# Optimization experiments

Hardware: AMD Instinct MI355X
Metric: run time of the kernel (lower is better)

The kernel has to match this reference:

```python
import jax, jax.numpy as jnp
import numpy as np

B, N, D, H = 2, 2048, 768, 12
HD = D // H  # 64


def apply_rotary_embed(x, thetas):
    # x: (..., N, HD), thetas: (N, HD) broadcast over leading dims
    x1, x2 = jnp.split(x, 2, axis=-1)
    x_rot = jnp.concatenate([-x2, x1], axis=-1)
    return x * jnp.cos(thetas) + x_rot * jnp.sin(thetas)


def setup_inputs() -> dict:
    key = jax.random.key(0)
    ks = jax.random.split(key, 5)
    s = 0.02
    return {
        "x": jax.random.normal(ks[0], (B, N, D), dtype=jnp.float32),
        "pos_embed": jax.random.normal(ks[1], (N, HD), dtype=jnp.float32),
        "Wqkv": jax.random.normal(ks[2], (3 * D, D), dtype=jnp.float32) * s,
        "Wproj": jax.random.normal(ks[3], (D, D), dtype=jnp.float32) * s,
        "bproj": jnp.zeros((D,), dtype=jnp.float32),
    }


def reference(x, pos_embed, Wqkv, Wproj, bproj):
    Bb, Nn, Dd = x.shape
    # fused QKV projection (torch Linear: x @ W.T), no bias
    qkv = jnp.einsum('bnd,ed->bne', x, Wqkv)                 # (B, N, 3D)
    qkv = qkv.reshape(Bb, Nn, 3, H, HD).transpose(2, 0, 3, 1, 4)  # (3, B, H, N, HD)
    q, k, v = qkv[0], qkv[1], qkv[2]
    # rotary embedding on q and k
    q = apply_rotary_embed(q, pos_embed)
    k = apply_rotary_embed(k, pos_embed)
    # scaled dot-product attention (non-causal, no mask, no dropout)
    scale = 1.0 / jnp.sqrt(jnp.asarray(HD, dtype=x.dtype))
    scores = jnp.einsum('bhqd,bhkd->bhqk', q, k) * scale     # (B, H, N, N)
    attn = jax.nn.softmax(scores, axis=-1)
    out = jnp.einsum('bhqk,bhkd->bhqd', attn, v)             # (B, H, N, HD)
    out = out.transpose(0, 2, 1, 3).reshape(Bb, Nn, Dd)      # (B, N, D)
    # output projection (with bias)
    return jnp.einsum('bnd,ed->bne', out, Wproj) + bproj
```

## Files before the change

kernel.cpp:

```cpp
#include <hip/hip_runtime.h>
#include <stdint.h>

typedef __attribute__((ext_vector_type(8))) short short8;
typedef __attribute__((ext_vector_type(4))) float floatx4;
typedef __attribute__((ext_vector_type(16))) float floatx16;
typedef __attribute__((ext_vector_type(4))) unsigned int uintx4;

#define BB 2
#define NN 2048
#define DD 768
#define HH 12
#define HDD 64
#define MM (BB*NN)

__device__ __forceinline__ unsigned short f2bf(float f) {
  unsigned int u = __builtin_bit_cast(unsigned int, f);
  u += 0x7fffu + ((u >> 16) & 1u);
  return (unsigned short)(u >> 16);
}
__device__ __forceinline__ float bf2f(unsigned short u) {
  unsigned int v = ((unsigned int)u) << 16;
  return __builtin_bit_cast(float, v);
}

__device__ __forceinline__ void gld16(const unsigned short* g, unsigned short* l) {
  __builtin_amdgcn_global_load_lds(
      (const __attribute__((address_space(1))) void*)g,
      (__attribute__((address_space(3))) void*)l, 16, 0, 0);
}

__device__ __forceinline__ unsigned int cvtpk_bf16(float a, float b) {
  unsigned int r;
  asm("v_cvt_pk_bf16_f32 %0, %1, %2" : "=v"(r) : "v"(a), "v"(b));
  return r;
}
__device__ __forceinline__ void plswap(unsigned int& a, unsigned int& b) {
  asm("v_permlane32_swap_b32 %0, %1" : "+v"(a), "+v"(b));
}

__global__ void cvt_all(const float* __restrict__ x, const float* __restrict__ wq,
                        const float* __restrict__ wp, const float* __restrict__ pos,
                        unsigned short* __restrict__ xb, unsigned short* __restrict__ wqb,
                        unsigned short* __restrict__ wpb, float* __restrict__ cst) {
  const int n1 = MM*DD/4, n2 = 3*DD*DD/4, n3 = DD*DD/4, n4 = NN*HDD/4;
  int i = blockIdx.x * blockDim.x + threadIdx.x;
  if (i >= n1+n2+n3) {
    int j = i - n1 - n2 - n3;
    if (j >= n4) return;
    float4 v = reinterpret_cast<const float4*>(pos)[j];
    float4 o0, o1;
    __sincosf(v.x, &o0.y, &o0.x);
    __sincosf(v.y, &o0.w, &o0.z);
    __sincosf(v.z, &o1.y, &o1.x);
    __sincosf(v.w, &o1.w, &o1.z);
    reinterpret_cast<float4*>(cst)[2*j]   = o0;
    reinterpret_cast<float4*>(cst)[2*j+1] = o1;
    return;
  }
  const float* s; unsigned short* d; int j;
  if (i < n1)            { s = x;  d = xb;  j = i; }
  else if (i < n1+n2)    { s = wq; d = wqb; j = i - n1; }
  else                   { s = wp; d = wpb; j = i - n1 - n2; }
  float4 v = reinterpret_cast<const float4*>(s)[j];
  unsigned int lo = (unsigned int)f2bf(v.x) | ((unsigned int)f2bf(v.y) << 16);
  unsigned int hi = (unsigned int)f2bf(v.z) | ((unsigned int)f2bf(v.w) << 16);
  reinterpret_cast<uint2*>(d)[j] = make_uint2(lo, hi);
}

template<int MODE, int MT, int NT, int BK>
__global__ __launch_bounds__(256) void gemm_bt(
    const unsigned short* __restrict__ A,
    const unsigned short* __restrict__ Bt,
    void* __restrict__ Cout, const float* __restrict__ bias,
    int Nn, int K,
    const float2* __restrict__ cst,
    unsigned short* __restrict__ qb2, unsigned short* __restrict__ kb2,
    unsigned short* __restrict__ vb2)
{
  constexpr int MTC = MT / 32;
  constexpr int NTC = NT / 32;
  constexpr int PARTS = BK / 8;
  __shared__ __align__(16) unsigned short as_[MT*BK];
  __shared__ __align__(16) unsigned short bs_[NT*BK];
  const int t = threadIdx.x;
  const int w = t >> 6, lane = t & 63;
  const int quad = lane >> 4, l16 = lane & 15;
  const int wm = (w >> 1) * (MT/2), wn = (w & 1) * (NT/2);
  const int m0 = blockIdx.y * MT, n0 = blockIdx.x * NT;

  const floatx4 fz = {0.f, 0.f, 0.f, 0.f};
  floatx4 acc[MTC][NTC];
#pragma unroll
  for (int mt = 0; mt < MTC; mt++)
#pragma unroll
    for (int nt = 0; nt < NTC; nt++) acc[mt][nt] = fz;

  for (int k0 = 0; k0 < K; k0 += BK) {
    __syncthreads();
#pragma unroll
    for (int i = 0; i < MT*PARTS/256; i++) {
      int c = t + i * 256;
      int row = c / PARTS, part = c % PARTS;
      int sp = part ^ (row & (PARTS-1));
      gld16(&A[(size_t)(m0 + row)*K + k0 + sp*8], &as_[c*8]);
    }
#pragma unroll
    for (int i = 0; i < NT*PARTS/256; i++) {
      int c = t + i * 256;
      int row = c / PARTS, part = c % PARTS;
      int sp = part ^ (row & (PARTS-1));
      gld16(&Bt[(size_t)(n0 + row)*K + k0 + sp*8], &bs_[c*8]);
    }
    __syncthreads();
#pragma unroll
    for (int kh = 0; kh < BK/32; kh++) {
      short8 af[MTC], bfr[NTC];
#pragma unroll
      for (int mt = 0; mt < MTC; mt++) {
        int row = wm + mt*16 + l16;
        int slot = (kh*4 + quad) ^ (row & (PARTS-1));
        af[mt] = *reinterpret_cast<const short8*>(&as_[row*BK + slot*8]);
      }
#pragma unroll
      for (int nt = 0; nt < NTC; nt++) {
        int row = wn + nt*16 + l16;
        int slot = (kh*4 + quad) ^ (row & (PARTS-1));
        bfr[nt] = *reinterpret_cast<const short8*>(&bs_[row*BK + slot*8]);
      }
#pragma unroll
      for (int mt = 0; mt < MTC; mt++)
#pragma unroll
        for (int nt = 0; nt < NTC; nt++)
          acc[mt][nt] = __builtin_amdgcn_mfma_f32_16x16x32_bf16(af[mt], bfr[nt], acc[mt][nt], 0, 0, 0);
    }
  }
  if (MODE == 2) {
    const int region = n0 / DD;
    const int nl0 = n0 - region * DD;
    const int head = (nl0 + wn) / HDD;
    if (region < 2) {
#pragma unroll
      for (int mt = 0; mt < MTC; mt++)
#pragma unroll
        for (int r = 0; r < 4; r++) {
          int gm = m0 + wm + mt*16 + quad*4 + r;
          int bq = gm >> 11, nseq = gm & (NN-1);
          size_t base = ((size_t)(bq*HH + head)*NN + nseq) * HDD;
#pragma unroll
          for (int nt = 0; nt < 2; nt++) {
            int hd = nt*16 + l16;
            float2 cs1 = cst[nseq*HDD + hd];
            float2 cs2 = cst[nseq*HDD + hd + 32];
            float c1 = cs1.x, s1 = cs1.y, c2 = cs2.x, s2 = cs2.y;
            float a1 = acc[mt][nt][r], a2 = acc[mt][nt+2][r];
            if (region == 0) {
              qb2[base + hd]      = f2bf((a1*c1 - a2*s1) * 0.125f);
              qb2[base + hd + 32] = f2bf((a2*c2 + a1*s2) * 0.125f);
            } else {
              int sl1 = (hd >> 3) ^ (nseq & 7);
              int sl2 = ((hd >> 3) + 4) ^ (nseq & 7);
              kb2[base + sl1*8 + (hd & 7)] = f2bf(a1*c1 - a2*s1);
              kb2[base + sl2*8 + (hd & 7)] = f2bf(a2*c2 + a1*s2);
            }
          }
        }
    } else {
#pragma unroll
      for (int mt = 0; mt < MTC; mt++)
#pragma unroll
        for (int nt = 0; nt < NTC; nt++) {
          int hd = nt*16 + l16;
          int seqb = m0 + wm + mt*16 + quad*4;
          int bq = seqb >> 11, nsb = seqb & (NN-1);
          unsigned int p0 = (unsigned int)f2bf(acc[mt][nt][0]) | ((unsigned int)f2bf(acc[mt][nt][1]) << 16);
          unsigned int p1 = (unsigned int)f2bf(acc[mt][nt][2]) | ((unsigned int)f2bf(acc[mt][nt][3]) << 16);
          int slot = ((nsb >> 3) & 15) ^ (hd & 7);
          size_t addr = ((size_t)(bq*HH + head)*HDD + hd) * NN + (nsb & ~127) + slot*8 + (nsb & 7);
          *(uint2*)&vb2[addr] = make_uint2(p0, p1);
        }
    }
  } else {
#pragma unroll
    for (int mt = 0; mt < MTC; mt++)
#pragma unroll
      for (int nt = 0; nt < NTC; nt++)
#pragma unroll
        for (int r = 0; r < 4; r++) {
          int gm = m0 + wm + mt*16 + quad*4 + r;
          int gn = n0 + wn + nt*16 + l16;
          float v = acc[mt][nt][r];
          if (MODE == 0)
            reinterpret_cast<unsigned short*>(Cout)[(size_t)gm * Nn + gn] = f2bf(v);
          else
            reinterpret_cast<float*>(Cout)[(size_t)gm * Nn + gn] = v + bias[gn];
        }
  }
}

__global__ __launch_bounds__(256, 4) void flash_attn(
    const unsigned short* __restrict__ qb, const unsigned short* __restrict__ kb,
    const unsigned short* __restrict__ vb, unsigned short* __restrict__ ob)
{
  __shared__ __align__(16) unsigned short smem[2*8192];
  __shared__ float lsd[128];
  const int qt = blockIdx.x, bh = blockIdx.y;
  const int b = bh / HH, hh = bh % HH;
  const int tid = threadIdx.x;
  const int w = tid >> 6, lane = tid & 63;
  const int l32 = lane & 31, hf = lane >> 5;
  const int gq = w >> 1;
  const int kh = w & 1;
  const int q0 = qt * 64;
  const size_t kbase = (size_t)bh * (NN*HDD);

  short8 qf[4];
  {
    const unsigned short* qp = &qb[((size_t)bh*NN + q0 + gq*32 + l32)*HDD + hf*8];
#pragma unroll
    for (int s = 0; s < 4; s++) qf[s] = *(const short8*)&qp[s*16];
  }
  floatx16 fz16;
#pragma unroll
  for (int z = 0; z < 16; z++) fz16[z] = 0.f;
  floatx16 oacc[2];
  oacc[0] = fz16; oacc[1] = fz16;
  float lrow = 0.f;

  auto stage = [&](int buf, int t) {
    unsigned short* kd = smem + buf*8192;
    unsigned short* vd = smem + buf*8192 + 4096;
#pragma unroll
    for (int i = 0; i < 2; i++) {
      int c = i*256 + tid;
      gld16(&kb[kbase + (size_t)(t*64 + (c >> 3))*64 + (c & 7)*8], &kd[c*8]);
    }
#pragma unroll
    for (int i = 0; i < 2; i++) {
      int c = i*256 + tid;
      gld16(&vb[kbase + (size_t)(c >> 3)*NN + t*64 + (c & 7)*8], &vd[c*8]);
    }
  };

  auto compute = [&](int buf) {
    const unsigned short* kc = smem + buf*8192;
    const unsigned short* vc = smem + buf*8192 + 4096;
    const int row = kh*32 + l32;
    floatx16 acc;
#pragma unroll
    for (int z = 0; z < 16; z++) acc[z] = 0.f;
    __builtin_amdgcn_s_setprio(1);
#pragma unroll
    for (int s = 0; s < 4; s++) {
      int cd = (2*s + hf) ^ (l32 & 7);
      short8 kf = *(const short8*)&kc[row*64 + cd*8];
      acc = __builtin_amdgcn_mfma_f32_32x32x16_bf16(kf, qf[s], acc, 0, 0, 0);
    }
    __builtin_amdgcn_s_setprio(0);
    float pv_[16];
    float rs = 0.f;
#pragma unroll
    for (int r = 0; r < 16; r++) { pv_[r] = __expf(acc[r]); rs += pv_[r]; }
    unsigned int w0 = cvtpk_bf16(pv_[0],  pv_[1]);
    unsigned int w1 = cvtpk_bf16(pv_[2],  pv_[3]);
    unsigned int w2 = cvtpk_bf16(pv_[4],  pv_[5]);
    unsigned int w3 = cvtpk_bf16(pv_[6],  pv_[7]);
    unsigned int w4 = cvtpk_bf16(pv_[8],  pv_[9]);
    unsigned int w5 = cvtpk_bf16(pv_[10], pv_[11]);
    unsigned int w6 = cvtpk_bf16(pv_[12], pv_[13]);
    unsigned int w7 = cvtpk_bf16(pv_[14], pv_[15]);
    plswap(w0, w2); plswap(w1, w3);
    plswap(w4, w6); plswap(w5, w7);
    uintx4 ua = {w0, w1, w2, w3};
    uintx4 ub = {w4, w5, w6, w7};
    short8 pfr0 = __builtin_bit_cast(short8, ua);
    short8 pfr1 = __builtin_bit_cast(short8, ub);
    rs += __shfl_xor(rs, 32);
    lrow += rs;
    __builtin_amdgcn_s_setprio(1);
#pragma unroll
    for (int ss = 0; ss < 2; ss++) {
      int ca = (kh*4 + ss*2 + hf) ^ (l32 & 7);
      short8 pf = ss ? pfr1 : pfr0;
#pragma unroll
      for (int ht = 0; ht < 2; ht++) {
        int hd = ht*32 + l32;
        short8 vf = *(const short8*)&vc[hd*64 + ca*8];
        oacc[ht] = __builtin_amdgcn_mfma_f32_32x32x16_bf16(pf, vf, oacc[ht], 0, 0, 0);
      }
    }
    __builtin_amdgcn_s_setprio(0);
  };

  stage(0, 0);
  __syncthreads();
  for (int t = 0; t < NN/64; t += 2) {
    if (t + 1 < NN/64) stage(1, t + 1);
    compute(0);
    __syncthreads();
    if (t + 2 < NN/64) stage(0, t + 2);
    compute(1);
    __syncthreads();
  }

  float* om = (float*)smem;
  if (kh) {
    float* base = om + gq*2048;
#pragma unroll
    for (int ht = 0; ht < 2; ht++)
#pragma unroll
      for (int g = 0; g < 4; g++)
#pragma unroll
        for (int e = 0; e < 4; e++) {
          int ql = hf*4 + g*8 + e;
          base[ql*64 + ht*32 + l32] = oacc[ht][4*g+e];
        }
  }
  if (hf == 0) lsd[w*32 + l32] = lrow;
  __syncthreads();
  if (!kh) {
    float* base = om + gq*2048;
#pragma unroll
    for (int g = 0; g < 4; g++)
#pragma unroll
      for (int e = 0; e < 4; e++) {
        int ql = hf*4 + g*8 + e;
        float l = lsd[gq*64 + ql] + lsd[gq*64 + 32 + ql];
        float inv = 1.f / l;
        int qrow = q0 + gq*32 + ql;
#pragma unroll
        for (int ht = 0; ht < 2; ht++) {
          float v = oacc[ht][4*g+e] + base[ql*64 + ht*32 + l32];
          ob[((size_t)(b*NN + qrow))*DD + hh*HDD + ht*32 + l32] = f2bf(v * inv);
        }
      }
  }
}

extern "C" void kernel_launch(void* const* d_in, const int* in_sizes, int n_in,
                              void* d_out, int out_size, void* d_ws, size_t ws_size,
                              hipStream_t stream)
{
  const float* x     = (const float*)d_in[0];
  const float* pos   = (const float*)d_in[1];
  const float* Wqkv  = (const float*)d_in[2];
  const float* Wproj = (const float*)d_in[3];
  const float* bproj = (const float*)d_in[4];

  unsigned short* p = (unsigned short*)d_ws;
  unsigned short* xb     = p; p += (size_t)MM*DD;
  unsigned short* wqkvb  = p; p += (size_t)3*DD*DD;
  unsigned short* wprojb = p; p += (size_t)DD*DD;
  unsigned short* ob     = p; p += (size_t)MM*DD;
  unsigned short* qb     = p; p += (size_t)BB*HH*NN*HDD;
  unsigned short* kb     = p; p += (size_t)BB*HH*NN*HDD;
  unsigned short* vb     = p; p += (size_t)BB*HH*NN*HDD;
  float* cst             = (float*)p; p += (size_t)NN*HDD*4;

  const int ncvt = MM*DD/4 + 3*DD*DD/4 + DD*DD/4 + NN*HDD/4;
  cvt_all<<<ncvt/256, 256, 0, stream>>>(x, Wqkv, Wproj, pos, xb, wqkvb, wprojb, cst);

  gemm_bt<2,64,128,64><<<dim3(3*DD/128, MM/64), 256, 0, stream>>>(
      xb, wqkvb, nullptr, nullptr, 3*DD, DD, (const float2*)cst, qb, kb, vb);
  flash_attn<<<dim3(NN/64, BB*HH), 256, 0, stream>>>(qb, kb, vb, ob);
  gemm_bt<1,64,64,64><<<dim3(DD/64, MM/64), 256, 0, stream>>>(
      ob, wprojb, (float*)d_out, bproj, DD, DD, nullptr, nullptr, nullptr, nullptr);
}
```

Baseline: 157.7 us.

## Double-buffer GEMM shared-memory tiles, swizzle block order, and shrink K tile

Both projection GEMMs now keep two LDS buffers per operand, so the async global-to-LDS loads for the next K tile are issued before the MFMA work on the current tile. This hides load latency and cuts one barrier per iteration. Work-group IDs are remapped with a stride-8 swizzle to change which tiles run together and improve cache locality. BK drops from 64 to 32, with the XOR swizzle adjusted to keep LDS accesses conflict-free. The smaller BK means more loop iterations and barriers per tile.

```diff
diff --git a/kernel.cpp b/kernel.cpp
--- a/kernel.cpp
+++ b/kernel.cpp
@@ -80,13 +80,19 @@
   constexpr int MTC = MT / 32;
   constexpr int NTC = NT / 32;
   constexpr int PARTS = BK / 8;
-  __shared__ __align__(16) unsigned short as_[MT*BK];
-  __shared__ __align__(16) unsigned short bs_[NT*BK];
+  constexpr int SH = (BK == 32) ? 1 : 0;
+  __shared__ __align__(16) unsigned short as_[2][MT*BK];
+  __shared__ __align__(16) unsigned short bs_[2][NT*BK];
   const int t = threadIdx.x;
   const int w = t >> 6, lane = t & 63;
   const int quad = lane >> 4, l16 = lane & 15;
   const int wm = (w >> 1) * (MT/2), wn = (w & 1) * (NT/2);
-  const int m0 = blockIdx.y * MT, n0 = blockIdx.x * NT;
+
+  const int nbx = gridDim.x;
+  const int nwg = nbx * gridDim.y;
+  const int bid = blockIdx.y * nbx + blockIdx.x;
+  const int swz = (bid & 7) * (nwg >> 3) + (bid >> 3);
+  const int m0 = (swz / nbx) * MT, n0 = (swz % nbx) * NT;
 
   const floatx4 fz = {0.f, 0.f, 0.f, 0.f};
   floatx4 acc[MTC][NTC];
@@ -95,37 +101,38 @@
 #pragma unroll
     for (int nt = 0; nt < NTC; nt++) acc[mt][nt] = fz;
 
-  for (int k0 = 0; k0 < K; k0 += BK) {
-    __syncthreads();
+  auto stage = [&](int buf, int k0) {
 #pragma unroll
     for (int i = 0; i < MT*PARTS/256; i++) {
       int c = t + i * 256;
       int row = c / PARTS, part = c % PARTS;
-      int sp = part ^ (row & (PARTS-1));
-      gld16(&A[(size_t)(m0 + row)*K + k0 + sp*8], &as_[c*8]);
+      int sp = part ^ ((row >> SH) & (PARTS-1));
+      gld16(&A[(size_t)(m0 + row)*K + k0 + sp*8], &as_[buf][c*8]);
     }
 #pragma unroll
     for (int i = 0; i < NT*PARTS/256; i++) {
       int c = t + i * 256;
       int row = c / PARTS, part = c % PARTS;
-      int sp = part ^ (row & (PARTS-1));
-      gld16(&Bt[(size_t)(n0 + row)*K + k0 + sp*8], &bs_[c*8]);
-    }
-    __syncthreads();
+      int sp = part ^ ((row >> SH) & (PARTS-1));
+      gld16(&Bt[(size_t)(n0 + row)*K + k0 + sp*8], &bs_[buf][c*8]);
+    }
+  };
+
+  auto compute_t = [&](int buf) {
 #pragma unroll
     for (int kh = 0; kh < BK/32; kh++) {
       short8 af[MTC], bfr[NTC];
 #pragma unroll
       for (int mt = 0; mt < MTC; mt++) {
         int row = wm + mt*16 + l16;
-        int slot = (kh*4 + quad) ^ (row & (PARTS-1));
-        af[mt] = *reinterpret_cast<const short8*>(&as_[row*BK + slot*8]);
+        int slot = (kh*4 + quad) ^ ((row >> SH) & (PARTS-1));
+        af[mt] = *reinterpret_cast<const short8*>(&as_[buf][row*BK + slot*8]);
       }
 #pragma unroll
       for (int nt = 0; nt < NTC; nt++) {
         int row = wn + nt*16 + l16;
-        int slot = (kh*4 + quad) ^ (row & (PARTS-1));
-        bfr[nt] = *reinterpret_cast<const short8*>(&bs_[row*BK + slot*8]);
+        int slot = (kh*4 + quad) ^ ((row >> SH) & (PARTS-1));
+        bfr[nt] = *reinterpret_cast<const short8*>(&bs_[buf][row*BK + slot*8]);
       }
 #pragma unroll
       for (int mt = 0; mt < MTC; mt++)
@@ -133,7 +140,19 @@
         for (int nt = 0; nt < NTC; nt++)
           acc[mt][nt] = __builtin_amdgcn_mfma_f32_16x16x32_bf16(af[mt], bfr[nt], acc[mt][nt], 0, 0, 0);
     }
-  }
+  };
+
+  stage(0, 0);
+  __syncthreads();
+  for (int k0 = 0; k0 < K; k0 += 2*BK) {
+    if (k0 + BK < K) stage(1, k0 + BK);
+    compute_t(0);
+    __syncthreads();
+    if (k0 + 2*BK < K) stage(0, k0 + 2*BK);
+    compute_t(1);
+    __syncthreads();
+  }
+
   if (MODE == 2) {
     const int region = n0 / DD;
     const int nl0 = n0 - region * DD;
@@ -359,9 +378,9 @@
   const int ncvt = MM*DD/4 + 3*DD*DD/4 + DD*DD/4 + NN*HDD/4;
   cvt_all<<<ncvt/256, 256, 0, stream>>>(x, Wqkv, Wproj, pos, xb, wqkvb, wprojb, cst);
 
-  gemm_bt<2,64,128,64><<<dim3(3*DD/128, MM/64), 256, 0, stream>>>(
+  gemm_bt<2,64,128,32><<<dim3(3*DD/128, MM/64), 256, 0, stream>>>(
       xb, wqkvb, nullptr, nullptr, 3*DD, DD, (const float2*)cst, qb, kb, vb);
   flash_attn<<<dim3(NN/64, BB*HH), 256, 0, stream>>>(qb, kb, vb, ob);
-  gemm_bt<1,64,64,64><<<dim3(DD/64, MM/64), 256, 0, stream>>>(
+  gemm_bt<1,64,64,32><<<dim3(DD/64, MM/64), 256, 0, stream>>>(
       ob, wprojb, (float*)d_out, bproj, DD, DD, nullptr, nullptr, nullptr, nullptr);
 }
```

Result: slower. 170.0 us (+7.8%).
